# Kernel optimization log

Measured on AMD Instinct MI355X. Metric: run time of the kernel, lower is better.

Reference implementation:

```python
import jax, jax.numpy as jnp
import numpy as np

EMBED_SIZE = 1024
HEADS = 16
HEAD_DIM = EMBED_SIZE // HEADS  # 64


def setup_inputs() -> dict:
    key = jax.random.key(0)
    k_x, k_q, k_k, k_v, k_o, k_b = jax.random.split(key, 6)
    B, S = 32, 8192  # S divisible by HEADS
    x = jax.random.normal(k_x, (B, S, HEAD_DIM), dtype=jnp.float32)
    # torch.nn.Linear weights are [out, in]; scale ~ 1/sqrt(fan_in)
    s_h = 1.0 / np.sqrt(HEAD_DIM)
    s_e = 1.0 / np.sqrt(EMBED_SIZE)
    Wq = jax.random.uniform(k_q, (HEAD_DIM, HEAD_DIM), jnp.float32, -s_h, s_h)
    Wk = jax.random.uniform(k_k, (HEAD_DIM, HEAD_DIM), jnp.float32, -s_h, s_h)
    Wv = jax.random.uniform(k_v, (HEAD_DIM, HEAD_DIM), jnp.float32, -s_h, s_h)
    Wo = jax.random.uniform(k_o, (EMBED_SIZE, EMBED_SIZE), jnp.float32, -s_e, s_e)
    bo = jax.random.uniform(k_b, (EMBED_SIZE,), jnp.float32, -s_e, s_e)
    return {"x": x, "Wq": Wq, "Wk": Wk, "Wv": Wv, "Wo": Wo, "bo": bo}


def reference(x, Wq, Wk, Wv, Wo, bo):
    B = x.shape[0]
    # Q/K/V projections: Linear(head_dim, head_dim), bias=False -> x @ W.T
    Q = (x @ Wq.T).reshape(B, -1, HEADS, HEAD_DIM)  # [B, G, H, D], G = S/H
    K = (x @ Wk.T).reshape(B, -1, HEADS, HEAD_DIM)
    V = (x @ Wv.T).reshape(B, -1, HEADS, HEAD_DIM)
    # energy = Q @ K^T over last two dims -> [B, G, H, H]
    energy = jnp.einsum('bghd,bgkd->bghk', Q, K)
    attn = jax.nn.softmax(energy / jnp.sqrt(jnp.float32(EMBED_SIZE)), axis=3)
    out = jnp.einsum('bghk,bgkd->bghd', attn, V)      # [B, G, H, D]
    out = out.transpose(0, 2, 1, 3).reshape(B, -1, EMBED_SIZE)  # [B, S/H, E]
    return out @ Wo.T + bo
```

## Files before the change

### kernel.cpp

```cpp
#include <hip/hip_runtime.h>
#include <hip/hip_bf16.h>
#include <stdint.h>

#define TOKS   262144
#define NGRP   16384
#define EMB    1024
#define HD     64

using bf16x8 = __attribute__((ext_vector_type(8))) short;
using f32x4  = __attribute__((ext_vector_type(4))) float;

__device__ __forceinline__ unsigned pack2(float a, float b) {
    union { __hip_bfloat162 h; unsigned u; } cvt;
    cvt.h = __float22bfloat162_rn(make_float2(a, b));
    return cvt.u;
}
__device__ __forceinline__ bf16x8 cvt8(float4 v0, float4 v1) {
    uint4 u;
    u.x = pack2(v0.x, v0.y);
    u.y = pack2(v0.z, v0.w);
    u.z = pack2(v1.x, v1.y);
    u.w = pack2(v1.z, v1.w);
    return __builtin_bit_cast(bf16x8, u);
}
__device__ __forceinline__ void gload_lds16(const unsigned short* g, unsigned short* l) {
    __builtin_amdgcn_global_load_lds(
        (const __attribute__((address_space(1))) void*)g,
        (__attribute__((address_space(3))) void*)l,
        16, 0, 0);
}

__global__ __launch_bounds__(256) void k_cvt(const float* __restrict__ wo,
                                             const float* __restrict__ wq,
                                             const float* __restrict__ wk,
                                             const float* __restrict__ wv,
                                             unsigned short* __restrict__ wob,
                                             unsigned short* __restrict__ wqkvb) {
    int bid = blockIdx.x;
    if (bid < 1024) {
        int idx = (bid * 256 + threadIdx.x) * 4;
        float4 v = *(const float4*)(wo + idx);
        uint2 p;
        p.x = pack2(v.x, v.y);
        p.y = pack2(v.z, v.w);
        *(uint2*)(wob + idx) = p;
    } else {
        int b = bid - 1024;
        int m = b >> 2;
        const float* src = (m == 0) ? wq : ((m == 1) ? wk : wv);
        int idx = ((b & 3) * 256 + threadIdx.x) * 4;
        float4 v = *(const float4*)(src + idx);
        uint2 p;
        p.x = pack2(v.x, v.y);
        p.y = pack2(v.z, v.w);
        *(uint2*)(wqkvb + m * 4096 + idx) = p;
    }
}

#define SCL 0.0450842200278f

__global__ __launch_bounds__(256) void k_fused(const float* __restrict__ x,
                                               const unsigned short* __restrict__ wqkv,
                                               unsigned short* __restrict__ out2) {
    __shared__ __align__(16) unsigned short qkls[4][2][2][16 * 72];
    int t = threadIdx.x;
    int w = t >> 6, l = t & 63;
    int c = l & 15, q = l >> 4;
    int waveTok0 = blockIdx.x * 128 + w * 32;

    bf16x8 xa[2][2];
    #pragma unroll
    for (int g = 0; g < 2; ++g) {
        const float* xp = x + (size_t)(waveTok0 + g * 16 + c) * 64 + q * 8;
        #pragma unroll
        for (int kc = 0; kc < 2; ++kc) {
            float4 v0 = *(const float4*)(xp + kc * 32);
            float4 v1 = *(const float4*)(xp + kc * 32 + 4);
            xa[g][kc] = cvt8(v0, v1);
        }
    }

    uint2 pkV[2][4];
    #pragma unroll
    for (int m = 0; m < 3; ++m) {
        #pragma unroll
        for (int nb = 0; nb < 4; ++nb) {
            const unsigned short* wp = wqkv + m * 4096 + (nb * 16 + c) * 64 + q * 8;
            bf16x8 w0 = *(const bf16x8*)(wp);
            bf16x8 w1 = *(const bf16x8*)(wp + 32);
            #pragma unroll
            for (int g = 0; g < 2; ++g) {
                f32x4 acc = (f32x4){0.f, 0.f, 0.f, 0.f};
                acc = __builtin_amdgcn_mfma_f32_16x16x32_bf16(xa[g][0], w0, acc, 0, 0, 0);
                acc = __builtin_amdgcn_mfma_f32_16x16x32_bf16(xa[g][1], w1, acc, 0, 0, 0);
                unsigned u01 = pack2(acc[0], acc[1]);
                unsigned u23 = pack2(acc[2], acc[3]);
                if (m < 2) {
                    unsigned short* tile = qkls[w][g][m];
                    int base = 4 * q * 72 + nb * 16 + c;
                    tile[base]       = (unsigned short)u01;
                    tile[base + 72]  = (unsigned short)(u01 >> 16);
                    tile[base + 144] = (unsigned short)u23;
                    tile[base + 216] = (unsigned short)(u23 >> 16);
                } else {
                    pkV[g][nb].x = u01;
                    pkV[g][nb].y = u23;
                }
            }
        }
    }

    f32x4 e[2];
    #pragma unroll
    for (int g = 0; g < 2; ++g) {
        const unsigned short* Qt = qkls[w][g][0];
        const unsigned short* Kt = qkls[w][g][1];
        e[g] = (f32x4){0.f, 0.f, 0.f, 0.f};
        #pragma unroll
        for (int kc = 0; kc < 2; ++kc) {
            bf16x8 ka = *(const bf16x8*)(Kt + c * 72 + kc * 32 + q * 8);
            bf16x8 qb = *(const bf16x8*)(Qt + c * 72 + kc * 32 + q * 8);
            e[g] = __builtin_amdgcn_mfma_f32_16x16x32_bf16(ka, qb, e[g], 0, 0, 0);
        }
    }

    unsigned pa0[2], pa1[2];
    #pragma unroll
    for (int g = 0; g < 2; ++g) {
        float mx = fmaxf(fmaxf(e[g][0], e[g][1]), fmaxf(e[g][2], e[g][3]));
        mx = fmaxf(mx, __shfl_xor(mx, 16));
        mx = fmaxf(mx, __shfl_xor(mx, 32));
        float p0 = exp2f((e[g][0] - mx) * SCL);
        float p1 = exp2f((e[g][1] - mx) * SCL);
        float p2 = exp2f((e[g][2] - mx) * SCL);
        float p3 = exp2f((e[g][3] - mx) * SCL);
        float s = p0 + p1 + p2 + p3;
        s += __shfl_xor(s, 16);
        s += __shfl_xor(s, 32);
        float rinv = 1.0f / s;
        pa0[g] = pack2(p0 * rinv, p1 * rinv);
        pa1[g] = pack2(p2 * rinv, p3 * rinv);
    }

    int s0 = (32 * q + c) & 63;
    int s1 = (32 * q + 16 + c) & 63;
    int v0 = 32 * (q & 1) + c;
    int v1 = v0 + 16;
    bool hi = (q >= 2);
    #pragma unroll
    for (int g = 0; g < 2; ++g) {
        int a0 = __shfl((int)pa0[g], s0);
        int a1 = __shfl((int)pa1[g], s0);
        int a2 = __shfl((int)pa0[g], s1);
        int a3 = __shfl((int)pa1[g], s1);
        uint4 A2u;
        A2u.x = hi ? 0u : (unsigned)a0;
        A2u.y = hi ? 0u : (unsigned)a1;
        A2u.z = hi ? 0u : (unsigned)a2;
        A2u.w = hi ? 0u : (unsigned)a3;
        bf16x8 A2 = __builtin_bit_cast(bf16x8, A2u);

        unsigned short* Ot = qkls[w][g][0];
        #pragma unroll
        for (int nb = 0; nb < 4; ++nb) {
            uint4 B2u;
            B2u.x = (unsigned)__shfl((int)pkV[g][nb].x, v0);
            B2u.y = (unsigned)__shfl((int)pkV[g][nb].y, v0);
            B2u.z = (unsigned)__shfl((int)pkV[g][nb].x, v1);
            B2u.w = (unsigned)__shfl((int)pkV[g][nb].y, v1);
            bf16x8 B2 = __builtin_bit_cast(bf16x8, B2u);
            f32x4 o = (f32x4){0.f, 0.f, 0.f, 0.f};
            o = __builtin_amdgcn_mfma_f32_16x16x32_bf16(A2, B2, o, 0, 0, 0);
            unsigned u01 = pack2(o[0], o[1]);
            unsigned u23 = pack2(o[2], o[3]);
            int base = 4 * q * 72 + nb * 16 + c;
            Ot[base]       = (unsigned short)u01;
            Ot[base + 72]  = (unsigned short)(u01 >> 16);
            Ot[base + 144] = (unsigned short)u23;
            Ot[base + 216] = (unsigned short)(u23 >> 16);
        }
    }

    #pragma unroll
    for (int g = 0; g < 2; ++g) {
        int gi = (waveTok0 >> 4) + g;
        int b    = gi >> 9;
        int grem = gi & 511;
        int rowbase = b * 512 + (grem >> 4);
        int colpref = (grem & 15) * 64;
        const unsigned short* osrc = qkls[w][g][0] + (l >> 2) * 72 + (l & 3) * 16;
        uint4 ov0 = *(const uint4*)(osrc);
        uint4 ov1 = *(const uint4*)(osrc + 8);
        unsigned short* dst = out2 + (size_t)(rowbase + (l >> 2) * 32) * 1024
                                   + colpref + (l & 3) * 16;
        *(uint4*)(dst)     = ov0;
        *(uint4*)(dst + 8) = ov1;
    }
}

#define STG(gb, lb, half, kt) do { \
    gload_lds16((gb) + (size_t)(half) * 131072 + (size_t)(kt) * 64 + ga0, \
                (lb) + (half) * 8192 + lo0); \
    gload_lds16((gb) + (size_t)(half) * 131072 + (size_t)(kt) * 64 + ga1, \
                (lb) + (half) * 8192 + lo1); \
} while (0)

#define LDA4(buf, mh) do { \
    _Pragma("unroll") \
    for (int i2 = 0; i2 < 4; ++i2) { \
        const unsigned short* _p = (buf) + (wrow + ((mh) * 4 + i2) * 16 + lm) * 64; \
        a[i2][0] = *(const bf16x8*)(_p + jo0); \
        a[i2][1] = *(const bf16x8*)(_p + jo1); \
    } \
} while (0)

#define LDB2(dst, buf, nh) do { \
    _Pragma("unroll") \
    for (int j2 = 0; j2 < 2; ++j2) { \
        const unsigned short* _p = (buf) + (wcol + ((nh) * 2 + j2) * 16 + lm) * 64; \
        dst[j2][0] = *(const bf16x8*)(_p + jo0); \
        dst[j2][1] = *(const bf16x8*)(_p + jo1); \
    } \
} while (0)

#define MM8(mh, nh, B) do { \
    _Pragma("unroll") \
    for (int i2 = 0; i2 < 4; ++i2) { \
        _Pragma("unroll") \
        for (int j2 = 0; j2 < 2; ++j2) { \
            acc[(mh)*4+i2][(nh)*2+j2] = __builtin_amdgcn_mfma_f32_16x16x32_bf16( \
                a[i2][0], B[j2][0], acc[(mh)*4+i2][(nh)*2+j2], 0, 0, 0); \
            acc[(mh)*4+i2][(nh)*2+j2] = __builtin_amdgcn_mfma_f32_16x16x32_bf16( \
                a[i2][1], B[j2][1], acc[(mh)*4+i2][(nh)*2+j2], 0, 0, 0); \
        } \
    } \
} while (0)

#define PHASE_MID() do { \
    __builtin_amdgcn_s_barrier(); \
    asm volatile("s_waitcnt lgkmcnt(0)" ::: "memory"); \
    __builtin_amdgcn_sched_barrier(0); \
    __builtin_amdgcn_s_setprio(1); \
} while (0)

#define PHASE_END() do { \
    __builtin_amdgcn_s_setprio(0); \
    __builtin_amdgcn_s_barrier(); \
} while (0)

__global__ __launch_bounds__(512, 2) void k_gemm256(const unsigned short* __restrict__ A,
                                                    const unsigned short* __restrict__ Bm,
                                                    const float* __restrict__ bias,
                                                    float* __restrict__ C) {
    extern __shared__ __align__(16) unsigned short lds[];
    unsigned short* As0 = lds;
    unsigned short* As1 = lds + 16384;
    unsigned short* Bs0 = lds + 32768;
    unsigned short* Bs1 = lds + 49152;

    const int t = threadIdx.x;
    const int w = t >> 6, l = t & 63;
    const int lm = l & 15, q4 = l >> 4;
    const int jxor = lm & 7;
    const int jo0 = ((0 + q4) ^ jxor) * 8;
    const int jo1 = ((4 + q4) ^ jxor) * 8;

    const int bid = blockIdx.x;
    const int wg  = (bid & 7) * 32 + (bid >> 3);
    const int m0  = (wg >> 2) * 256;
    const int n0  = (wg & 3) * 256;

    const int wrow = (w >> 2) * 128;
    const int wcol = (w & 3) * 64;

    const int s1 = w * 128 + l;
    const int s2 = s1 + 64;
    const int r0 = s1 >> 3, c0 = s1 & 7;
    const int r1 = s2 >> 3, c1 = s2 & 7;
    const size_t ga0 = (size_t)r0 * 1024 + (size_t)((c0 ^ (r0 & 7)) * 8);
    const size_t ga1 = (size_t)r1 * 1024 + (size_t)((c1 ^ (r1 & 7)) * 8);
    const int lo0 = s1 * 8;
    const int lo1 = s2 * 8;

    const unsigned short* Ab = A  + (size_t)m0 * 1024;
    const unsigned short* Bb = Bm + (size_t)n0 * 1024;

    f32x4 acc[8][4];
    #pragma unroll
    for (int mi = 0; mi < 8; ++mi)
        #pragma unroll
        for (int ni = 0; ni < 4; ++ni)
            acc[mi][ni] = (f32x4){0.f, 0.f, 0.f, 0.f};

    bf16x8 a[4][2], b0[2][2], b1[2][2];

    STG(Ab, As0, 0, 0); STG(Ab, As0, 1, 0);
    STG(Bb, Bs0, 0, 0); STG(Bb, Bs0, 1, 0);
    STG(Bb, Bs1, 0, 1); STG(Bb, Bs1, 1, 1);
    asm volatile("s_waitcnt vmcnt(4)" ::: "memory");
    __builtin_amdgcn_s_barrier();

    #pragma unroll 1
    for (int it = 0; it < 8; ++it) {
        const int kt1 = 2 * it + 1;
        const int kt2 = 2 * it + 2;
        const int kt3 = 2 * it + 3;
        const bool more = (it < 7);

        LDA4(As0, 0); LDB2(b0, Bs0, 0);
        STG(Ab, As1, 0, kt1);
        PHASE_MID(); MM8(0, 0, b0); PHASE_END();

        LDB2(b1, Bs0, 1);
        STG(Ab, As1, 1, kt1);
        PHASE_MID(); MM8(0, 1, b1); PHASE_END();

        LDA4(As0, 1);
        if (more) STG(Bb, Bs0, 0, kt2);
        PHASE_MID(); MM8(1, 1, b1); PHASE_END();

        if (more) STG(Bb, Bs0, 1, kt2);
        PHASE_MID(); MM8(1, 0, b0);
        __builtin_amdgcn_s_setprio(0);
        if (more) { asm volatile("s_waitcnt vmcnt(4)" ::: "memory"); }
        else      { asm volatile("s_waitcnt vmcnt(0)" ::: "memory"); }
        __builtin_amdgcn_s_barrier();

        LDA4(As1, 0); LDB2(b0, Bs1, 0);
        if (more) STG(Ab, As0, 0, kt2);
        PHASE_MID(); MM8(0, 0, b0); PHASE_END();

        LDB2(b1, Bs1, 1);
        if (more) STG(Ab, As0, 1, kt2);
        PHASE_MID(); MM8(0, 1, b1); PHASE_END();

        LDA4(As1, 1);
        if (more) STG(Bb, Bs1, 0, kt3);
        PHASE_MID(); MM8(1, 1, b1); PHASE_END();

        if (more) STG(Bb, Bs1, 1, kt3);
        PHASE_MID(); MM8(1, 0, b0);
        __builtin_amdgcn_s_setprio(0);
        if (more) { asm volatile("s_waitcnt vmcnt(4)" ::: "memory"); }
        __builtin_amdgcn_s_barrier();
    }

    #pragma unroll
    for (int ni = 0; ni < 4; ++ni) {
        const int col = n0 + wcol + ni * 16 + lm;
        const float bcol = bias[col];
        #pragma unroll
        for (int mi = 0; mi < 8; ++mi) {
            #pragma unroll
            for (int r = 0; r < 4; ++r) {
                const int row = m0 + wrow + mi * 16 + q4 * 4 + r;
                C[(size_t)row * 1024 + col] = acc[mi][ni][r] + bcol;
            }
        }
    }
}

extern "C" void kernel_launch(void* const* d_in, const int* in_sizes, int n_in,
                              void* d_out, int out_size, void* d_ws, size_t ws_size,
                              hipStream_t stream) {
    const float* x  = (const float*)d_in[0];
    const float* wq = (const float*)d_in[1];
    const float* wk = (const float*)d_in[2];
    const float* wv = (const float*)d_in[3];
    const float* wo = (const float*)d_in[4];
    const float* bo = (const float*)d_in[5];
    float* out = (float*)d_out;

    unsigned short* out2  = (unsigned short*)d_ws;
    unsigned short* wob   = out2 + (size_t)NGRP * 1024;
    unsigned short* wqkvb = wob + (size_t)EMB * EMB;

    static int s_once = []() {
        hipFuncSetAttribute((const void*)k_gemm256,
                            hipFuncAttributeMaxDynamicSharedMemorySize, 131072);
        return 0;
    }();
    (void)s_once;

    k_cvt    <<<1036, 256, 0, stream>>>(wo, wq, wk, wv, wob, wqkvb);
    k_fused  <<<2048, 256, 0, stream>>>(x, wqkvb, out2);
    k_gemm256<<<256, 512, 131072, stream>>>(out2, wob, bo, out);
}
```

Measured before the change: 177.1 us.

## Load Wo B-operand directly from pre-swizzled global layout into registers, triple-buffer A

The weight-conversion kernel now writes Wo in bf16 in an MFMA-fragment-friendly packed layout. The output GEMM then loads B fragments straight from global or L2 into registers, double-buffered across k-tiles, rather than staging them through LDS. LDS is used only for A, with a rotating triple buffer, which shrinks shared memory from 128KB to 96KB. This removes LDS traffic and staging for B, at the cost of extra global loads per wave and more registers for the B buffers.

```diff
diff --git a/kernel.cpp b/kernel.cpp
--- a/kernel.cpp
+++ b/kernel.cpp
@@ -37,15 +37,19 @@
                                              unsigned short* __restrict__ wob,
                                              unsigned short* __restrict__ wqkvb) {
     int bid = blockIdx.x;
-    if (bid < 1024) {
-        int idx = (bid * 256 + threadIdx.x) * 4;
-        float4 v = *(const float4*)(wo + idx);
-        uint2 p;
-        p.x = pack2(v.x, v.y);
-        p.y = pack2(v.z, v.w);
-        *(uint2*)(wob + idx) = p;
+    if (bid < 512) {
+        int tid = bid * 256 + threadIdx.x;
+        int c   = tid >> 12;
+        int nb  = (tid >> 6) & 63;
+        int l   = tid & 63;
+        int n   = nb * 16 + (l & 15);
+        int k   = c * 32 + (l >> 4) * 8;
+        const float* src = wo + (size_t)n * 1024 + k;
+        float4 v0 = *(const float4*)(src);
+        float4 v1 = *(const float4*)(src + 4);
+        *(bf16x8*)(wob + (size_t)tid * 8) = cvt8(v0, v1);
     } else {
-        int b = bid - 1024;
+        int b = bid - 512;
         int m = b >> 2;
         const float* src = (m == 0) ? wq : ((m == 1) ? wk : wv);
         int idx = ((b & 3) * 256 + threadIdx.x) * 4;
@@ -214,12 +218,14 @@
     } \
 } while (0)
 
-#define LDB2(dst, buf, nh) do { \
+#define GLBB(d0, d1, gp) do { \
     _Pragma("unroll") \
-    for (int j2 = 0; j2 < 2; ++j2) { \
-        const unsigned short* _p = (buf) + (wcol + ((nh) * 2 + j2) * 16 + lm) * 64; \
-        dst[j2][0] = *(const bf16x8*)(_p + jo0); \
-        dst[j2][1] = *(const bf16x8*)(_p + jo1); \
+    for (int kc = 0; kc < 2; ++kc) { \
+        _Pragma("unroll") \
+        for (int j2 = 0; j2 < 2; ++j2) { \
+            d0[j2][kc] = *(const bf16x8*)((gp) + kc * 32768 + j2 * 512); \
+            d1[j2][kc] = *(const bf16x8*)((gp) + kc * 32768 + (2 + j2) * 512); \
+        } \
     } \
 } while (0)
 
@@ -248,15 +254,37 @@
     __builtin_amdgcn_s_barrier(); \
 } while (0)
 
+#define TILE(t, c0, c1, n0_, n1_) do { \
+    const int _t = (t); \
+     \
+    LDA4(pAr, 0); \
+    if (_t < 15) GLBB(n0_, n1_, gB); \
+    PHASE_MID(); MM8(0, 0, c0); PHASE_END(); \
+     \
+    if (_t < 14) STG(Ab, pAs, 0, _t + 2); \
+    PHASE_MID(); MM8(0, 1, c1); PHASE_END(); \
+     \
+    LDA4(pAr, 1); \
+    if (_t < 14) STG(Ab, pAs, 1, _t + 2); \
+    PHASE_MID(); MM8(1, 1, c1); PHASE_END(); \
+     \
+    PHASE_MID(); MM8(1, 0, c0); \
+    __builtin_amdgcn_s_setprio(0); \
+    if (_t < 14)       { asm volatile("s_waitcnt vmcnt(4)" ::: "memory"); } \
+    else if (_t == 14) { asm volatile("s_waitcnt vmcnt(0)" ::: "memory"); } \
+    __builtin_amdgcn_s_barrier(); \
+    unsigned short* _tmp = pAr; pAr = pAn; pAn = pAs; pAs = _tmp; \
+    gB += 65536; \
+} while (0)
+
 __global__ __launch_bounds__(512, 2) void k_gemm256(const unsigned short* __restrict__ A,
-                                                    const unsigned short* __restrict__ Bm,
+                                                    const unsigned short* __restrict__ Bp,
                                                     const float* __restrict__ bias,
                                                     float* __restrict__ C) {
     extern __shared__ __align__(16) unsigned short lds[];
     unsigned short* As0 = lds;
     unsigned short* As1 = lds + 16384;
-    unsigned short* Bs0 = lds + 32768;
-    unsigned short* Bs1 = lds + 49152;
+    unsigned short* As2 = lds + 32768;
 
     const int t = threadIdx.x;
     const int w = t >> 6, l = t & 63;
@@ -282,8 +310,9 @@
     const int lo0 = s1 * 8;
     const int lo1 = s2 * 8;
 
-    const unsigned short* Ab = A  + (size_t)m0 * 1024;
-    const unsigned short* Bb = Bm + (size_t)n0 * 1024;
+    const unsigned short* Ab = A + (size_t)m0 * 1024;
+    const unsigned short* gB = Bp + (size_t)((n0 >> 4) + (wcol >> 4)) * 512
+                                  + (size_t)l * 8;
 
     f32x4 acc[8][4];
     #pragma unroll
@@ -292,70 +321,38 @@
         for (int ni = 0; ni < 4; ++ni)
             acc[mi][ni] = (f32x4){0.f, 0.f, 0.f, 0.f};
 
-    bf16x8 a[4][2], b0[2][2], b1[2][2];
-
-    STG(Ab, As0, 0, 0); STG(Ab, As0, 1, 0);
-    STG(Bb, Bs0, 0, 0); STG(Bb, Bs0, 1, 0);
-    STG(Bb, Bs1, 0, 1); STG(Bb, Bs1, 1, 1);
+    unsigned short* pAr = As0;
+    unsigned short* pAn = As1;
+    unsigned short* pAs = As2;
+
+    bf16x8 a[4][2];
+    bf16x8 bE0[2][2], bE1[2][2], bO0[2][2], bO1[2][2];
+
+    GLBB(bE0, bE1, gB);
+    STG(Ab, pAr, 0, 0); STG(Ab, pAr, 1, 0);
+    STG(Ab, pAn, 0, 1); STG(Ab, pAn, 1, 1);
     asm volatile("s_waitcnt vmcnt(4)" ::: "memory");
     __builtin_amdgcn_s_barrier();
+    gB += 65536;
 
     #pragma unroll 1
-    for (int it = 0; it < 8; ++it) {
-        const int kt1 = 2 * it + 1;
-        const int kt2 = 2 * it + 2;
-        const int kt3 = 2 * it + 3;
-        const bool more = (it < 7);
-
-        LDA4(As0, 0); LDB2(b0, Bs0, 0);
-        STG(Ab, As1, 0, kt1);
-        PHASE_MID(); MM8(0, 0, b0); PHASE_END();
-
-        LDB2(b1, Bs0, 1);
-        STG(Ab, As1, 1, kt1);
-        PHASE_MID(); MM8(0, 1, b1); PHASE_END();
-
-        LDA4(As0, 1);
-        if (more) STG(Bb, Bs0, 0, kt2);
-        PHASE_MID(); MM8(1, 1, b1); PHASE_END();
-
-        if (more) STG(Bb, Bs0, 1, kt2);
-        PHASE_MID(); MM8(1, 0, b0);
-        __builtin_amdgcn_s_setprio(0);
-        if (more) { asm volatile("s_waitcnt vmcnt(4)" ::: "memory"); }
-        else      { asm volatile("s_waitcnt vmcnt(0)" ::: "memory"); }
-        __builtin_amdgcn_s_barrier();
-
-        LDA4(As1, 0); LDB2(b0, Bs1, 0);
-        if (more) STG(Ab, As0, 0, kt2);
-        PHASE_MID(); MM8(0, 0, b0); PHASE_END();
-
-        LDB2(b1, Bs1, 1);
-        if (more) STG(Ab, As0, 1, kt2);
-        PHASE_MID(); MM8(0, 1, b1); PHASE_END();
-
-        LDA4(As1, 1);
-        if (more) STG(Bb, Bs1, 0, kt3);
-        PHASE_MID(); MM8(1, 1, b1); PHASE_END();
-
-        if (more) STG(Bb, Bs1, 1, kt3);
-        PHASE_MID(); MM8(1, 0, b0);
-        __builtin_amdgcn_s_setprio(0);
-        if (more) { asm volatile("s_waitcnt vmcnt(4)" ::: "memory"); }
-        __builtin_amdgcn_s_barrier();
-    }
-
-    #pragma unroll
-    for (int ni = 0; ni < 4; ++ni) {
-        const int col = n0 + wcol + ni * 16 + lm;
-        const float bcol = bias[col];
-        #pragma unroll
-        for (int mi = 0; mi < 8; ++mi) {
+    for (int tt = 0; tt < 8; ++tt) {
+        TILE(2 * tt,     bE0, bE1, bO0, bO1);
+        TILE(2 * tt + 1, bO0, bO1, bE0, bE1);
+    }
+
+    float bc[4];
+    #pragma unroll
+    for (int ni = 0; ni < 4; ++ni) bc[ni] = bias[n0 + wcol + ni * 16 + lm];
+    #pragma unroll
+    for (int mi = 0; mi < 8; ++mi) {
+        #pragma unroll
+        for (int r = 0; r < 4; ++r) {
+            const int row = m0 + wrow + mi * 16 + q4 * 4 + r;
+            float* cp = C + (size_t)row * 1024 + n0 + wcol + lm;
             #pragma unroll
-            for (int r = 0; r < 4; ++r) {
-                const int row = m0 + wrow + mi * 16 + q4 * 4 + r;
-                C[(size_t)row * 1024 + col] = acc[mi][ni][r] + bcol;
-            }
+            for (int ni = 0; ni < 4; ++ni)
+                cp[ni * 16] = acc[mi][ni][r] + bc[ni];
         }
     }
 }
@@ -377,12 +374,12 @@
 
     static int s_once = []() {
         hipFuncSetAttribute((const void*)k_gemm256,
-                            hipFuncAttributeMaxDynamicSharedMemorySize, 131072);
+                            hipFuncAttributeMaxDynamicSharedMemorySize, 98304);
         return 0;
     }();
     (void)s_once;
 
-    k_cvt    <<<1036, 256, 0, stream>>>(wo, wq, wk, wv, wob, wqkvb);
+    k_cvt    <<<524,  256, 0, stream>>>(wo, wq, wk, wv, wob, wqkvb);
     k_fused  <<<2048, 256, 0, stream>>>(x, wqkvb, out2);
-    k_gemm256<<<256, 512, 131072, stream>>>(out2, wob, bo, out);
-}
+    k_gemm256<<<256, 512, 98304, stream>>>(out2, wob, bo, out);
+}
```

Result: no change. 177.8 us (+0.4%).
